# Performance work log

Measured on AMD Instinct MI355X. Metric: run time of the kernel, lower is better.

The kernel has to match this reference:

```python
import jax, jax.numpy as jnp
import numpy as np

B, T, C = 2, 2048, 1024
NH, NKV, HD, NG = 16, 8, 64, 8   # heads, kv heads, head_dim, global heads
NG_KV = NG * NKV // NH           # global kv heads = 4
VE_CH = 32                       # ve_gate input channels
WIN = 1024                       # local sliding-window (left) size


def setup_inputs() -> dict:
    key = jax.random.key(0)
    ks = jax.random.split(key, 8)
    x = jax.random.normal(ks[0], (B, T, C), jnp.float32)
    ve = jax.random.normal(ks[1], (B, T, NKV * HD), jnp.float32)
    # true rotary tables over half the head dim
    half = HD // 2
    inv_freq = 1.0 / (10000.0 ** (np.arange(half, dtype=np.float64) / half))
    ang = np.arange(T, dtype=np.float64)[:, None] * inv_freq[None, :]
    cos = jnp.asarray(np.cos(ang), jnp.float32)[None, :, None, :]  # [1,T,1,32]
    sin = jnp.asarray(np.sin(ang), jnp.float32)[None, :, None, :]
    s = C ** -0.5
    Wq = jax.random.normal(ks[2], (C, NH * HD), jnp.float32) * s
    Wk = jax.random.normal(ks[3], (C, NKV * HD), jnp.float32) * s
    Wv = jax.random.normal(ks[4], (C, NKV * HD), jnp.float32) * s
    Wproj = jax.random.normal(ks[5], (C, C), jnp.float32) * s
    Wg = jax.random.normal(ks[6], (VE_CH, NKV), jnp.float32) * (VE_CH ** -0.5)
    return dict(x=x, ve=ve, cos=cos, sin=sin, Wq=Wq, Wk=Wk, Wv=Wv,
                Wproj=Wproj, Wg=Wg, window=WIN)


def _rope(x, cos, sin):
    d = x.shape[-1] // 2
    x1, x2 = x[..., :d], x[..., d:]
    return jnp.concatenate([x1 * cos + x2 * sin, -x1 * sin + x2 * cos], axis=-1)


def _rms_norm(x):
    eps = jnp.asarray(jnp.finfo(x.dtype).eps, x.dtype)
    return x * jax.lax.rsqrt(jnp.mean(x * x, axis=-1, keepdims=True) + eps)


def _gqa_attn(q, k, v, left_window):
    # q: [B,T,Hq,D]; k,v: [B,T,Hk,D]; GQA with g = Hq//Hk queries per kv head.
    b, t, hq, d = q.shape
    hk = k.shape[2]
    g = hq // hk
    qg = q.reshape(b, t, hk, g, d)
    scores = jnp.einsum('bqhgd,bkhd->bhgqk', qg, k) * (d ** -0.5)
    i = jnp.arange(t)[:, None]
    j = jnp.arange(t)[None, :]
    if left_window < 0:
        mask = j <= i                       # full causal
    else:
        mask = (j <= i) & ((i - j) <= left_window)  # causal sliding window
    scores = jnp.where(mask, scores, jnp.asarray(-1e30, scores.dtype))
    p = jax.nn.softmax(scores, axis=-1)
    out = jnp.einsum('bhgqk,bkhd->bqhgd', p, v)
    return out.reshape(b, t, hq, d)


def reference(x, ve, cos, sin, Wq, Wk, Wv, Wproj, Wg, window):
    b, t, c = x.shape
    q = (x @ Wq).reshape(b, t, NH, HD)
    k = (x @ Wk).reshape(b, t, NKV, HD)
    v = (x @ Wv).reshape(b, t, NKV, HD)
    # value-embedding gating: gate = 2*sigmoid(Linear(x[..., :32])) per kv head
    gate = 2.0 * jax.nn.sigmoid(x[..., :VE_CH] @ Wg)       # [B,T,NKV]
    v = v + gate[..., None] * ve.reshape(b, t, NKV, HD)
    # inline RoPE then RMSNorm on q and k
    q = _rms_norm(_rope(q, cos, sin))
    k = _rms_norm(_rope(k, cos, sin))
    # split global (full causal) vs local (windowed) head groups
    y_global = _gqa_attn(q[:, :, :NG], k[:, :, :NG_KV], v[:, :, :NG_KV], -1)
    y_local = _gqa_attn(q[:, :, NG:], k[:, :, NG_KV:], v[:, :, NG_KV:], window)
    y = jnp.concatenate([y_global, y_local], axis=2).reshape(b, t, c)
    return y @ Wproj
```

## Files before the change

kernel.cpp:

```cpp
#include <hip/hip_runtime.h>
#include <hip/hip_bf16.h>
#include <math.h>

typedef __bf16 bf16x8 __attribute__((ext_vector_type(8)));
typedef __bf16 bf16x4 __attribute__((ext_vector_type(4)));
typedef float  f32x4  __attribute__((ext_vector_type(4)));

#define MFMA16(a, b, c) __builtin_amdgcn_mfma_f32_16x16x32_bf16((a), (b), (c), 0, 0, 0)

__device__ __forceinline__ void gload16(const void* g, void* lds) {
    __builtin_amdgcn_global_load_lds(
        (const __attribute__((address_space(1))) uint32_t*)g,
        (__attribute__((address_space(3))) uint32_t*)lds, 16, 0, 0);
}

__global__ __launch_bounds__(256)
void prep_kernel(const float* __restrict__ x, __bf16* __restrict__ xb,
                 const float* __restrict__ Wg, float* __restrict__ gate) {
    const int bx = blockIdx.x;
    if (bx < 4096) {
        int i = bx * 256 + threadIdx.x;
        float4 v = reinterpret_cast<const float4*>(x)[i];
        bf16x4 o = { (__bf16)v.x, (__bf16)v.y, (__bf16)v.z, (__bf16)v.w };
        *reinterpret_cast<bf16x4*>(xb + (size_t)i * 4) = o;
    } else {
        int idx = (bx - 4096) * 256 + threadIdx.x;
        int row = idx >> 3, j = idx & 7;
        float z = 0.f;
        #pragma unroll
        for (int i = 0; i < 32; ++i)
            z = fmaf(x[(size_t)row * 1024 + i], Wg[i * 8 + j], z);
        gate[idx] = 2.0f / (1.0f + expf(-z));
    }
}

__global__ __launch_bounds__(256)
void tw_all(const float* __restrict__ Wq, const float* __restrict__ Wk,
            const float* __restrict__ Wv, const float* __restrict__ Wproj,
            __bf16* __restrict__ wqkvt, __bf16* __restrict__ wprojt) {
    __shared__ __bf16 Ts[64 * 72];
    const int z = blockIdx.z;
    const float* W = (z == 0) ? Wq : (z == 1) ? Wk : (z == 2) ? Wv : Wproj;
    __bf16* dst = (z == 3) ? wprojt : wqkvt;
    const int N = (z == 1 || z == 2) ? 512 : 1024;
    const int nt_off = (z == 1) ? 1024 : (z == 2) ? 1536 : 0;
    const int n0 = blockIdx.x * 64, k0 = blockIdx.y * 64;
    if (n0 >= N) return;
    const int tid = threadIdx.x;
    {
        int r = tid >> 2;
        int c0 = (tid & 3) * 16;
        const float4* s4 = reinterpret_cast<const float4*>(
            W + (size_t)(k0 + r) * N + n0 + c0);
        float val[16];
        #pragma unroll
        for (int q = 0; q < 4; ++q) {
            float4 v = s4[q];
            val[q * 4 + 0] = v.x; val[q * 4 + 1] = v.y;
            val[q * 4 + 2] = v.z; val[q * 4 + 3] = v.w;
        }
        #pragma unroll
        for (int j = 0; j < 16; ++j) Ts[(c0 + j) * 72 + r] = (__bf16)val[j];
    }
    __syncthreads();
    {
        int n = tid >> 2, kg = (tid & 3) * 16;
        __bf16* out = dst + (size_t)(nt_off + n0 + n) * 1024 + k0 + kg;
        bf16x8 t0 = *reinterpret_cast<const bf16x8*>(&Ts[n * 72 + kg]);
        bf16x8 t1 = *reinterpret_cast<const bf16x8*>(&Ts[n * 72 + kg + 8]);
        *reinterpret_cast<bf16x8*>(out) = t0;
        *reinterpret_cast<bf16x8*>(out + 8) = t1;
    }
}

template <typename OutT>
__global__ __launch_bounds__(256)
void gemm_bf16(const __bf16* __restrict__ A, const __bf16* __restrict__ Bt,
               OutT* __restrict__ C, int M, int N, int K) {
    __shared__ __align__(16) __bf16 As[128 * 64];
    __shared__ __align__(16) __bf16 Bs[128 * 64];
    const int tid = threadIdx.x;
    const int lane = tid & 63, w = tid >> 6;
    const int wr = w >> 1, wc = w & 1;
    const int nwg = gridDim.x * gridDim.y;
    const int id = blockIdx.y * gridDim.x + blockIdx.x;
    const int nid = (id & 7) * (nwg >> 3) + (id >> 3);
    const int bxs = nid % gridDim.x, bys = nid / gridDim.x;
    const int bm = bys * 128, bn = bxs * 128;
    const int lhi = lane >> 4, llo = lane & 15;
    const int gsrc = (lane & 7) ^ ((lane >> 3) & 7);

    f32x4 acc[4][4] = {};

    for (int k0 = 0; k0 < K; k0 += 64) {
        __syncthreads();
        const __bf16* Ab = A + (size_t)bm * K + k0;
        const __bf16* Bb = Bt + (size_t)bn * K + k0;
        #pragma unroll
        for (int rr = 0; rr < 4; ++rr) {
            int c = rr * 4 + w;
            int r = c * 8 + (lane >> 3);
            gload16(Ab + (size_t)r * K + gsrc * 8, (char*)As + c * 1024);
            gload16(Bb + (size_t)r * K + gsrc * 8, (char*)Bs + c * 1024);
        }
        __syncthreads();

        #pragma unroll
        for (int ks = 0; ks < 2; ++ks) {
            bf16x8 af[4], bfr[4];
            int g = ks * 4 + lhi;
            #pragma unroll
            for (int i = 0; i < 4; ++i) {
                int ra = wr * 64 + i * 16 + llo;
                af[i] = *reinterpret_cast<const bf16x8*>(
                    (const char*)As + ra * 128 + ((g ^ (ra & 7)) << 4));
                int rb = wc * 64 + i * 16 + llo;
                bfr[i] = *reinterpret_cast<const bf16x8*>(
                    (const char*)Bs + rb * 128 + ((g ^ (rb & 7)) << 4));
            }
            #pragma unroll
            for (int i = 0; i < 4; ++i)
                #pragma unroll
                for (int j = 0; j < 4; ++j)
                    acc[i][j] = MFMA16(af[i], bfr[j], acc[i][j]);
        }
    }

    #pragma unroll
    for (int i = 0; i < 4; ++i) {
        #pragma unroll
        for (int j = 0; j < 4; ++j) {
            int col = bn + wc * 64 + j * 16 + llo;
            #pragma unroll
            for (int r = 0; r < 4; ++r) {
                int row = bm + wr * 64 + i * 16 + lhi * 4 + r;
                C[(size_t)row * N + col] = (OutT)acc[i][j][r];
            }
        }
    }
}

__global__ __launch_bounds__(256)
void post_kernel(__bf16* __restrict__ qkv, const float* __restrict__ ve,
                 const float* __restrict__ gate, const float* __restrict__ cosb,
                 const float* __restrict__ sinb, __bf16* __restrict__ vT) {
    const int id = blockIdx.x;
    const int tid = threadIdx.x;
    if (id < 24576) {
        const int u = id >> 10;
        const int row = (id & 1023) * 4 + (tid >> 6);
        const int d = tid & 63;
        const int t = row & 2047;
        const int off = (u < 16) ? u * 64 : 1024 + (u - 16) * 64;
        __bf16* p = qkv + (size_t)row * 2048 + off;
        float v = (float)p[d];
        float partner = __shfl(v, d ^ 32, 64);
        float r;
        if (d < 32) {
            float cs = cosb[t * 32 + d], sn = sinb[t * 32 + d];
            r = v * cs + partner * sn;
        } else {
            float cs = cosb[t * 32 + d - 32], sn = sinb[t * 32 + d - 32];
            r = -partner * sn + v * cs;
        }
        float s = r * r;
        #pragma unroll
        for (int mm = 1; mm < 64; mm <<= 1) s += __shfl_xor(s, mm, 64);
        r *= rsqrtf(s * (1.0f / 64.0f) + 1.1920929e-07f);
        if (u < 16) r *= 0.18033688011116012f;
        p[d] = (__bf16)r;
    } else {
        __shared__ __bf16 Ts[64 * 72];
        const int rem = id - 24576;
        const int ch = rem & 63;
        const int h = rem >> 6;
        {
            int r = tid >> 2, c0 = (tid & 3) * 16;
            int grow = ch * 64 + r;
            float g = gate[grow * 8 + h];
            const __bf16* vp = qkv + (size_t)grow * 2048 + 1536 + h * 64 + c0;
            const float* vep = ve + (size_t)grow * 512 + h * 64 + c0;
            bf16x8 v0 = *reinterpret_cast<const bf16x8*>(vp);
            bf16x8 v1 = *reinterpret_cast<const bf16x8*>(vp + 8);
            #pragma unroll
            for (int j = 0; j < 8; ++j) {
                Ts[(c0 + j) * 72 + r]     = (__bf16)((float)v0[j] + g * vep[j]);
                Ts[(c0 + 8 + j) * 72 + r] = (__bf16)((float)v1[j] + g * vep[8 + j]);
            }
        }
        __syncthreads();
        {
            int d = tid >> 2, t0l = (tid & 3) * 16;
            int b = ch >> 5, tloc = (ch & 31) * 64;
            __bf16* out = vT + ((size_t)((b * 8 + h) * 64 + d)) * 2048 + tloc + t0l;
            bf16x8 t0 = *reinterpret_cast<const bf16x8*>(&Ts[d * 72 + t0l]);
            bf16x8 t1 = *reinterpret_cast<const bf16x8*>(&Ts[d * 72 + t0l + 8]);
            *reinterpret_cast<bf16x8*>(out) = t0;
            *reinterpret_cast<bf16x8*>(out + 8) = t1;
        }
    }
}

__global__ __launch_bounds__(256, 4)
void attn_mfma(const __bf16* __restrict__ qkv, const __bf16* __restrict__ vT,
               __bf16* __restrict__ y, const int* __restrict__ winp) {
    __shared__ __align__(16) __bf16 Ks[2][64 * 64];
    __shared__ __align__(16) __bf16 VTs[2][64 * 64];
    __shared__ __align__(16) __bf16 Ps[4][16 * 64];

    const int bid = blockIdx.x;
    const int kvh = bid & 7;
    int tdec = bid >> 3;
    const int b = tdec & 1; tdec >>= 1;
    const int qh = tdec & 1;
    const int qt = 31 - (tdec >> 1);
    const int h = (kvh < 4) ? (kvh * 2 + qh) : (8 + (kvh - 4) * 2 + qh);
    const int q0 = qt * 64;
    const int tid = threadIdx.x, lane = tid & 63, w = tid >> 6;
    const int lhi = lane >> 4, llo = lane & 15;
    const int gsrc = (lane & 7) ^ ((lane >> 3) & 7);
    const int win = (h < 8) ? -1 : winp[0];
    const int winv = (win < 0) ? (1 << 30) : win;

    const __bf16* kbase = qkv + (size_t)(b * 2048) * 2048 + 1024 + kvh * 64;
    const __bf16* vtbase = vT + ((size_t)((b * 8 + kvh) * 64)) * 2048;

    int kts = 0;
    if (win >= 0) { int s = q0 - win; if (s > 0) kts = s >> 6; }

    const __bf16* qrow = qkv + (size_t)(b * 2048 + q0 + w * 16 + llo) * 2048
                         + h * 64 + lhi * 8;
    bf16x8 qf[2];
    qf[0] = *(const bf16x8*)(qrow);
    qf[1] = *(const bf16x8*)(qrow + 32);

    auto STAGE = [&](int buf, int ktx) {
        #pragma unroll
        for (int rr = 0; rr < 2; ++rr) {
            int c = rr * 4 + w;
            int r = c * 8 + (lane >> 3);
            gload16(kbase + (size_t)(ktx * 64 + r) * 2048 + gsrc * 8,
                    (char*)&Ks[buf][0] + c * 1024);
            gload16(vtbase + (size_t)r * 2048 + ktx * 64 + gsrc * 8,
                    (char*)&VTs[buf][0] + c * 1024);
        }
    };

    f32x4 oaccT[4] = {};
    float lrow = 0.f;
    int cur = 0;
    STAGE(0, kts);

    const int pswz = (llo & 7) << 4;

    for (int kt = kts; kt <= qt; ++kt) {
        __syncthreads();
        if (kt < qt) STAGE(cur ^ 1, kt + 1);

        f32x4 sacc[4] = {};
        __builtin_amdgcn_s_setprio(1);
        #pragma unroll
        for (int ks = 0; ks < 2; ++ks) {
            #pragma unroll
            for (int kj = 0; kj < 4; ++kj) {
                int rb = kj * 16 + llo;
                bf16x8 bk = *(const bf16x8*)((const char*)&Ks[cur][0]
                    + rb * 128 + (((ks * 4 + lhi) ^ (rb & 7)) << 4));
                sacc[kj] = MFMA16(bk, qf[ks], sacc[kj]);
            }
        }
        __builtin_amdgcn_s_setprio(0);

        const bool needMask = (kt == qt) || (win >= 0 && kt * 64 < q0 + 63 - winv);

        float sv[16];
        #pragma unroll
        for (int kj = 0; kj < 4; ++kj)
            #pragma unroll
            for (int r = 0; r < 4; ++r)
                sv[kj * 4 + r] = sacc[kj][r];
        if (needMask) {
            int qrowi = q0 + w * 16 + llo;
            #pragma unroll
            for (int kj = 0; kj < 4; ++kj)
                #pragma unroll
                for (int r = 0; r < 4; ++r) {
                    int key = kt * 64 + kj * 16 + lhi * 4 + r;
                    bool ok = (key <= qrowi) && (qrowi - key <= winv);
                    if (!ok) sv[kj * 4 + r] = -__builtin_inff();
                }
        }

        float p[16], rs = 0.f;
        #pragma unroll
        for (int t = 0; t < 16; ++t) {
            p[t] = __builtin_amdgcn_exp2f(sv[t] - 12.0f);
            rs += p[t];
        }
        lrow += rs;

        #pragma unroll
        for (int kj = 0; kj < 4; ++kj) {
            bf16x4 pk = { (__bf16)p[kj * 4 + 0], (__bf16)p[kj * 4 + 1],
                          (__bf16)p[kj * 4 + 2], (__bf16)p[kj * 4 + 3] };
            *(bf16x4*)((char*)&Ps[w][0]
                + ((llo * 128 + kj * 32 + lhi * 8) ^ pswz)) = pk;
        }

        __builtin_amdgcn_s_setprio(1);
        #pragma unroll
        for (int ks = 0; ks < 2; ++ks) {
            bf16x8 ap = *(const bf16x8*)((const char*)&Ps[w][0]
                + ((llo * 128 + ks * 64 + lhi * 16) ^ pswz));
            #pragma unroll
            for (int dj = 0; dj < 4; ++dj) {
                int rv = dj * 16 + llo;
                bf16x8 bv = *(const bf16x8*)((const char*)&VTs[cur][0]
                    + rv * 128 + (((ks * 4 + lhi) ^ (rv & 7)) << 4));
                oaccT[dj] = MFMA16(bv, ap, oaccT[dj]);
            }
        }
        __builtin_amdgcn_s_setprio(0);
        cur ^= 1;
    }

    lrow += __shfl_xor(lrow, 16, 64);
    lrow += __shfl_xor(lrow, 32, 64);

    float inv = 1.0f / lrow;
    int row = b * 2048 + q0 + w * 16 + llo;
    #pragma unroll
    for (int dj = 0; dj < 4; ++dj) {
        bf16x4 o = { (__bf16)(oaccT[dj][0] * inv), (__bf16)(oaccT[dj][1] * inv),
                     (__bf16)(oaccT[dj][2] * inv), (__bf16)(oaccT[dj][3] * inv) };
        *(bf16x4*)(&y[(size_t)row * 1024 + h * 64 + dj * 16 + lhi * 4]) = o;
    }
}

extern "C" void kernel_launch(void* const* d_in, const int* in_sizes, int n_in,
                              void* d_out, int out_size, void* d_ws, size_t ws_size,
                              hipStream_t stream) {
    const float* x     = (const float*)d_in[0];
    const float* ve    = (const float*)d_in[1];
    const float* cosb  = (const float*)d_in[2];
    const float* sinb  = (const float*)d_in[3];
    const float* Wq    = (const float*)d_in[4];
    const float* Wk    = (const float*)d_in[5];
    const float* Wv    = (const float*)d_in[6];
    const float* Wproj = (const float*)d_in[7];
    const float* Wg    = (const float*)d_in[8];
    const int*   winp  = (const int*)d_in[9];

    char* ws = (char*)d_ws;
    __bf16* qkv    = (__bf16*)(ws);
    __bf16* vT     = (__bf16*)(ws + (16u << 20));
    __bf16* ybuf   = (__bf16*)(ws + (20u << 20));
    __bf16* xb     = (__bf16*)(ws + (28u << 20));
    __bf16* wqkvt  = (__bf16*)(ws + (36u << 20));
    __bf16* wprojt = (__bf16*)(ws + (40u << 20));
    float*  gate   = (float*) (ws + (42u << 20));

    prep_kernel<<<4224, 256, 0, stream>>>(x, xb, Wg, gate);
    tw_all<<<dim3(16, 16, 4), 256, 0, stream>>>(Wq, Wk, Wv, Wproj, wqkvt, wprojt);
    gemm_bf16<__bf16><<<dim3(16, 32), 256, 0, stream>>>(xb, wqkvt, qkv, 4096, 2048, 1024);
    post_kernel<<<25088, 256, 0, stream>>>(qkv, ve, gate, cosb, sinb, vT);
    attn_mfma<<<1024, 256, 0, stream>>>(qkv, vT, ybuf, winp);
    gemm_bf16<float><<<dim3(8, 32), 256, 0, stream>>>(ybuf, wprojt, (float*)d_out, 4096, 1024, 1024);
}
```

Measured before the change: 119.5 us.

## Double attention query tile to 128 rows per block for K/V reuse

Each attention block now handles 128 query rows instead of 64, with each wave computing two 16-row sub-tiles that share the same K and V fragments loaded from LDS. This halves the global K/V staging traffic per query row and cuts the grid to 512 blocks. Block scheduling also changes so batch 1 runs tiles in reverse order, pairing heavy and light causal tiles. The cost is more registers (launch bounds drop to 3 waves per SIMD), a larger P buffer, fewer blocks for load balance, and extra masked work on the diagonal tiles.

```diff
diff --git a/kernel.cpp b/kernel.cpp
--- a/kernel.cpp
+++ b/kernel.cpp
@@ -201,21 +201,22 @@
     }
 }
 
-__global__ __launch_bounds__(256, 4)
+__global__ __launch_bounds__(256, 3)
 void attn_mfma(const __bf16* __restrict__ qkv, const __bf16* __restrict__ vT,
                __bf16* __restrict__ y, const int* __restrict__ winp) {
     __shared__ __align__(16) __bf16 Ks[2][64 * 64];
     __shared__ __align__(16) __bf16 VTs[2][64 * 64];
-    __shared__ __align__(16) __bf16 Ps[4][16 * 64];
+    __shared__ __align__(16) __bf16 Ps[4][32 * 64];
 
     const int bid = blockIdx.x;
     const int kvh = bid & 7;
-    int tdec = bid >> 3;
-    const int b = tdec & 1; tdec >>= 1;
-    const int qh = tdec & 1;
-    const int qt = 31 - (tdec >> 1);
+    const int u = bid >> 3;
+    const int b = u >> 5;
+    const int lo = u & 31;
+    const int qt4 = lo >> 1, qh = lo & 1;
+    const int qt = b ? (15 - qt4) : qt4;
     const int h = (kvh < 4) ? (kvh * 2 + qh) : (8 + (kvh - 4) * 2 + qh);
-    const int q0 = qt * 64;
+    const int q0 = qt * 128;
     const int tid = threadIdx.x, lane = tid & 63, w = tid >> 6;
     const int lhi = lane >> 4, llo = lane & 15;
     const int gsrc = (lane & 7) ^ ((lane >> 3) & 7);
@@ -227,12 +228,15 @@
 
     int kts = 0;
     if (win >= 0) { int s = q0 - win; if (s > 0) kts = s >> 6; }
-
-    const __bf16* qrow = qkv + (size_t)(b * 2048 + q0 + w * 16 + llo) * 2048
+    const int ktend = 2 * qt + 1;
+
+    const __bf16* qrow = qkv + (size_t)(b * 2048 + q0 + w * 32 + llo) * 2048
                          + h * 64 + lhi * 8;
-    bf16x8 qf[2];
-    qf[0] = *(const bf16x8*)(qrow);
-    qf[1] = *(const bf16x8*)(qrow + 32);
+    bf16x8 qf[2][2];
+    qf[0][0] = *(const bf16x8*)(qrow);
+    qf[0][1] = *(const bf16x8*)(qrow + 32);
+    qf[1][0] = *(const bf16x8*)(qrow + 16 * 2048);
+    qf[1][1] = *(const bf16x8*)(qrow + 16 * 2048 + 32);
 
     auto STAGE = [&](int buf, int ktx) {
         #pragma unroll
@@ -246,94 +250,115 @@
         }
     };
 
-    f32x4 oaccT[4] = {};
-    float lrow = 0.f;
+    f32x4 oaccT[2][4] = {};
+    float lrow[2] = {0.f, 0.f};
     int cur = 0;
     STAGE(0, kts);
 
     const int pswz = (llo & 7) << 4;
 
-    for (int kt = kts; kt <= qt; ++kt) {
+    for (int kt = kts; kt <= ktend; ++kt) {
         __syncthreads();
-        if (kt < qt) STAGE(cur ^ 1, kt + 1);
-
-        f32x4 sacc[4] = {};
+        if (kt < ktend) STAGE(cur ^ 1, kt + 1);
+
+        bf16x8 bk[4][2];
+        #pragma unroll
+        for (int kj = 0; kj < 4; ++kj) {
+            int rb = kj * 16 + llo;
+            #pragma unroll
+            for (int ks = 0; ks < 2; ++ks)
+                bk[kj][ks] = *(const bf16x8*)((const char*)&Ks[cur][0]
+                    + rb * 128 + (((ks * 4 + lhi) ^ (rb & 7)) << 4));
+        }
+        f32x4 sacc[2][4] = {};
         __builtin_amdgcn_s_setprio(1);
         #pragma unroll
+        for (int ks = 0; ks < 2; ++ks)
+            #pragma unroll
+            for (int mi = 0; mi < 2; ++mi)
+                #pragma unroll
+                for (int kj = 0; kj < 4; ++kj)
+                    sacc[mi][kj] = MFMA16(bk[kj][ks], qf[mi][ks], sacc[mi][kj]);
+        __builtin_amdgcn_s_setprio(0);
+
+        const bool needMask = (kt >= 2 * qt) ||
+                              (win >= 0 && kt * 64 < q0 + 127 - winv);
+
+        #pragma unroll
+        for (int mi = 0; mi < 2; ++mi) {
+            float sv[16];
+            #pragma unroll
+            for (int kj = 0; kj < 4; ++kj)
+                #pragma unroll
+                for (int r = 0; r < 4; ++r)
+                    sv[kj * 4 + r] = sacc[mi][kj][r];
+            if (needMask) {
+                int qrowi = q0 + w * 32 + mi * 16 + llo;
+                #pragma unroll
+                for (int kj = 0; kj < 4; ++kj)
+                    #pragma unroll
+                    for (int r = 0; r < 4; ++r) {
+                        int key = kt * 64 + kj * 16 + lhi * 4 + r;
+                        bool ok = (key <= qrowi) && (qrowi - key <= winv);
+                        if (!ok) sv[kj * 4 + r] = -__builtin_inff();
+                    }
+            }
+            float p[16], rs = 0.f;
+            #pragma unroll
+            for (int t = 0; t < 16; ++t) {
+                p[t] = __builtin_amdgcn_exp2f(sv[t] - 12.0f);
+                rs += p[t];
+            }
+            lrow[mi] += rs;
+            #pragma unroll
+            for (int kj = 0; kj < 4; ++kj) {
+                bf16x4 pk = { (__bf16)p[kj * 4 + 0], (__bf16)p[kj * 4 + 1],
+                              (__bf16)p[kj * 4 + 2], (__bf16)p[kj * 4 + 3] };
+                *(bf16x4*)((char*)&Ps[w][0]
+                    + (((mi * 16 + llo) * 128 + kj * 32 + lhi * 8) ^ pswz)) = pk;
+            }
+        }
+
+        __builtin_amdgcn_s_setprio(1);
+        #pragma unroll
         for (int ks = 0; ks < 2; ++ks) {
-            #pragma unroll
-            for (int kj = 0; kj < 4; ++kj) {
-                int rb = kj * 16 + llo;
-                bf16x8 bk = *(const bf16x8*)((const char*)&Ks[cur][0]
-                    + rb * 128 + (((ks * 4 + lhi) ^ (rb & 7)) << 4));
-                sacc[kj] = MFMA16(bk, qf[ks], sacc[kj]);
-            }
-        }
-        __builtin_amdgcn_s_setprio(0);
-
-        const bool needMask = (kt == qt) || (win >= 0 && kt * 64 < q0 + 63 - winv);
-
-        float sv[16];
-        #pragma unroll
-        for (int kj = 0; kj < 4; ++kj)
-            #pragma unroll
-            for (int r = 0; r < 4; ++r)
-                sv[kj * 4 + r] = sacc[kj][r];
-        if (needMask) {
-            int qrowi = q0 + w * 16 + llo;
-            #pragma unroll
-            for (int kj = 0; kj < 4; ++kj)
-                #pragma unroll
-                for (int r = 0; r < 4; ++r) {
-                    int key = kt * 64 + kj * 16 + lhi * 4 + r;
-                    bool ok = (key <= qrowi) && (qrowi - key <= winv);
-                    if (!ok) sv[kj * 4 + r] = -__builtin_inff();
-                }
-        }
-
-        float p[16], rs = 0.f;
-        #pragma unroll
-        for (int t = 0; t < 16; ++t) {
-            p[t] = __builtin_amdgcn_exp2f(sv[t] - 12.0f);
-            rs += p[t];
-        }
-        lrow += rs;
-
-        #pragma unroll
-        for (int kj = 0; kj < 4; ++kj) {
-            bf16x4 pk = { (__bf16)p[kj * 4 + 0], (__bf16)p[kj * 4 + 1],
-                          (__bf16)p[kj * 4 + 2], (__bf16)p[kj * 4 + 3] };
-            *(bf16x4*)((char*)&Ps[w][0]
-                + ((llo * 128 + kj * 32 + lhi * 8) ^ pswz)) = pk;
-        }
-
-        __builtin_amdgcn_s_setprio(1);
-        #pragma unroll
-        for (int ks = 0; ks < 2; ++ks) {
-            bf16x8 ap = *(const bf16x8*)((const char*)&Ps[w][0]
-                + ((llo * 128 + ks * 64 + lhi * 16) ^ pswz));
+            bf16x8 ap[2];
+            #pragma unroll
+            for (int mi = 0; mi < 2; ++mi)
+                ap[mi] = *(const bf16x8*)((const char*)&Ps[w][0]
+                    + (((mi * 16 + llo) * 128 + ks * 64 + lhi * 16) ^ pswz));
             #pragma unroll
             for (int dj = 0; dj < 4; ++dj) {
                 int rv = dj * 16 + llo;
                 bf16x8 bv = *(const bf16x8*)((const char*)&VTs[cur][0]
                     + rv * 128 + (((ks * 4 + lhi) ^ (rv & 7)) << 4));
-                oaccT[dj] = MFMA16(bv, ap, oaccT[dj]);
+                #pragma unroll
+                for (int mi = 0; mi < 2; ++mi)
+                    oaccT[mi][dj] = MFMA16(bv, ap[mi], oaccT[mi][dj]);
             }
         }
         __builtin_amdgcn_s_setprio(0);
         cur ^= 1;
     }
 
-    lrow += __shfl_xor(lrow, 16, 64);
-    lrow += __shfl_xor(lrow, 32, 64);
-
-    float inv = 1.0f / lrow;
-    int row = b * 2048 + q0 + w * 16 + llo;
     #pragma unroll
-    for (int dj = 0; dj < 4; ++dj) {
-        bf16x4 o = { (__bf16)(oaccT[dj][0] * inv), (__bf16)(oaccT[dj][1] * inv),
-                     (__bf16)(oaccT[dj][2] * inv), (__bf16)(oaccT[dj][3] * inv) };
-        *(bf16x4*)(&y[(size_t)row * 1024 + h * 64 + dj * 16 + lhi * 4]) = o;
+    for (int mi = 0; mi < 2; ++mi) {
+        lrow[mi] += __shfl_xor(lrow[mi], 16, 64);
+        lrow[mi] += __shfl_xor(lrow[mi], 32, 64);
+    }
+
+    #pragma unroll
+    for (int mi = 0; mi < 2; ++mi) {
+        float inv = 1.0f / lrow[mi];
+        int row = b * 2048 + q0 + w * 32 + mi * 16 + llo;
+        #pragma unroll
+        for (int dj = 0; dj < 4; ++dj) {
+            bf16x4 o = { (__bf16)(oaccT[mi][dj][0] * inv),
+                         (__bf16)(oaccT[mi][dj][1] * inv),
+                         (__bf16)(oaccT[mi][dj][2] * inv),
+                         (__bf16)(oaccT[mi][dj][3] * inv) };
+            *(bf16x4*)(&y[(size_t)row * 1024 + h * 64 + dj * 16 + lhi * 4]) = o;
+        }
     }
 }
 
@@ -364,6 +389,6 @@
     tw_all<<<dim3(16, 16, 4), 256, 0, stream>>>(Wq, Wk, Wv, Wproj, wqkvt, wprojt);
     gemm_bf16<__bf16><<<dim3(16, 32), 256, 0, stream>>>(xb, wqkvt, qkv, 4096, 2048, 1024);
     post_kernel<<<25088, 256, 0, stream>>>(qkv, ve, gate, cosb, sinb, vT);
-    attn_mfma<<<1024, 256, 0, stream>>>(qkv, vT, ybuf, winp);
+    attn_mfma<<<512, 256, 0, stream>>>(qkv, vT, ybuf, winp);
     gemm_bf16<float><<<dim3(8, 32), 256, 0, stream>>>(ybuf, wprojt, (float*)d_out, 4096, 1024, 1024);
 }
```

Result: slower. 131.4 us (+9.9%).
